# Performance work log

Hardware: AMD Instinct MI355X
Metric: run time of the kernel (lower is better)

The kernel has to match this reference:

```python
import jax, jax.numpy as jnp
import numpy as np

N_NODES = 50000
N_EDGES = 800000
IN_DIM = 128
HID = 64
N_GRAPHS = 256


def setup_inputs() -> dict:
    key = jax.random.key(0)
    ks = jax.random.split(key, 10)
    s = lambda d: 1.0 / np.sqrt(d)
    return {
        'x': jax.random.normal(ks[0], (N_NODES, IN_DIM), jnp.float32),
        'edge_index': jax.random.randint(ks[1], (2, N_EDGES), 0, N_NODES, jnp.int64),
        'batch': jnp.sort(jax.random.randint(ks[2], (N_NODES,), 0, N_GRAPHS, jnp.int64)),
        'Wp': jax.random.normal(ks[3], (IN_DIM, HID), jnp.float32) * s(IN_DIM),
        'bp': jnp.zeros((HID,), jnp.float32),
        'W1_0': jax.random.normal(ks[4], (HID, HID), jnp.float32) * s(HID),
        'b1_0': jnp.zeros((HID,), jnp.float32),
        'W2_0': jax.random.normal(ks[5], (HID, HID), jnp.float32) * s(HID),
        'b2_0': jnp.zeros((HID,), jnp.float32),
        'W1_1': jax.random.normal(ks[6], (HID, HID), jnp.float32) * s(HID),
        'b1_1': jnp.zeros((HID,), jnp.float32),
        'W2_1': jax.random.normal(ks[7], (HID, HID), jnp.float32) * s(HID),
        'b2_1': jnp.zeros((HID,), jnp.float32),
    }


def _gin_layer(h, src, dst, W1, b1, W2, b2):
    # scatter-add aggregation: sum_{j in N(i)} h_j  (messages flow src -> dst)
    agg = jax.ops.segment_sum(h[src], dst, num_segments=N_NODES)
    z = h + agg  # eps = 0 (GINConv default)
    z = jax.nn.relu(z @ W1 + b1)
    z = z @ W2 + b2
    return jax.nn.relu(z)  # outer activation from SharedGINEncoder


def reference(x, edge_index, batch, Wp, bp, W1_0, b1_0, W2_0, b2_0, W1_1, b1_1, W2_1, b2_1):
    src, dst = edge_index[0], edge_index[1]
    h = jax.nn.relu(x @ Wp + bp)  # [N, HID]
    h = _gin_layer(h, src, dst, W1_0, b1_0, W2_0, b2_0)
    h = _gin_layer(h, src, dst, W1_1, b1_1, W2_1, b2_1)
    # global_mean_pool over graph ids
    sums = jax.ops.segment_sum(h, batch, num_segments=N_GRAPHS)  # [G, HID]
    counts = jax.ops.segment_sum(jnp.ones((h.shape[0],), h.dtype), batch, num_segments=N_GRAPHS)
    return sums / jnp.maximum(counts, 1.0)[:, None]
```

## Files before the change

### kernel.cpp

```cpp
#include <hip/hip_runtime.h>

#define N_NODES 50000
#define N_EDGES 800000
#define IN_DIM 128
#define HID 64
#define N_GRAPHS 256

#define E_PER_BLK 4000
#define F_BLOCKS (N_EDGES / E_PER_BLK)
#define NBKT ((N_NODES + 255) / 256)
#define CNT_N (NBKT * F_BLOCKS)
#define SCB ((CNT_N + 255) / 256)
#define NTILES (N_NODES / 4)
#define MTILES (N_NODES / 16)


__device__ __forceinline__ float bf2f(unsigned short v) {
  return __uint_as_float(((unsigned int)v) << 16);
}
__device__ __forceinline__ unsigned short f2bf(float f) {
  unsigned int u = __float_as_uint(f);
  return (unsigned short)((u + 0x7fffu + ((u >> 16) & 1u)) >> 16);
}

typedef __attribute__((ext_vector_type(8))) short bf16x8;
typedef __attribute__((ext_vector_type(4))) float f32x4;

__global__ __launch_bounds__(256) void part_hist_kernel(const int* __restrict__ dst,
                                                        int* __restrict__ cnt) {
  __shared__ int h[NBKT];
  const int t = threadIdx.x;
  for (int k = t; k < NBKT; k += 256) h[k] = 0;
  __syncthreads();
  const int base = blockIdx.x * E_PER_BLK;
  for (int i = t; i < E_PER_BLK; i += 256) atomicAdd(&h[dst[base + i] >> 8], 1);
  __syncthreads();
  for (int k = t; k < NBKT; k += 256) cnt[k * F_BLOCKS + blockIdx.x] = h[k];
}

__global__ __launch_bounds__(256) void scan1g_kernel(const int* __restrict__ in,
                                                     int* __restrict__ ex,
                                                     int* __restrict__ bsum, int n) {
  __shared__ int s[256];
  const int t = threadIdx.x;
  const int i = blockIdx.x * 256 + t;
  int v = (i < n) ? in[i] : 0;
  s[t] = v;
  __syncthreads();
#pragma unroll
  for (int ofs = 1; ofs < 256; ofs <<= 1) {
    int u = (t >= ofs) ? s[t - ofs] : 0;
    __syncthreads();
    s[t] += u;
    __syncthreads();
  }
  if (i < n) ex[i] = s[t] - v;
  if (t == 255) bsum[blockIdx.x] = s[255];
}

__global__ __launch_bounds__(256) void scan2g_kernel(const int* __restrict__ bsum,
                                                     int* __restrict__ bpref, int nb) {
  __shared__ int s[256];
  const int t = threadIdx.x;
  int v = (t < nb) ? bsum[t] : 0;
  s[t] = v;
  __syncthreads();
#pragma unroll
  for (int ofs = 1; ofs < 256; ofs <<= 1) {
    int u = (t >= ofs) ? s[t - ofs] : 0;
    __syncthreads();
    s[t] += u;
    __syncthreads();
  }
  if (t < nb) bpref[t] = s[t] - v;
}

__global__ __launch_bounds__(256) void scan3g_kernel(int* __restrict__ ex,
                                                     const int* __restrict__ bpref, int n) {
  const int i = blockIdx.x * 256 + threadIdx.x;
  if (i < n) ex[i] += bpref[blockIdx.x];
}

__global__ __launch_bounds__(256) void part_scatter_kernel(const int* __restrict__ src,
                                                           const int* __restrict__ dst,
                                                           const int* __restrict__ cex,
                                                           int* __restrict__ psrc,
                                                           int* __restrict__ pdst) {
  __shared__ int cur[NBKT];
  const int t = threadIdx.x;
  for (int k = t; k < NBKT; k += 256) cur[k] = cex[k * F_BLOCKS + blockIdx.x];
  __syncthreads();
  const int base = blockIdx.x * E_PER_BLK;
  for (int i = t; i < E_PER_BLK; i += 256) {
    int d = dst[base + i], s = src[base + i];
    int p = atomicAdd(&cur[d >> 8], 1);
    pdst[p] = d;
    psrc[p] = s;
  }
}

__global__ __launch_bounds__(256) void bucket_sort_kernel(const int* __restrict__ psrc,
                                                          const int* __restrict__ pdst,
                                                          const int* __restrict__ cex,
                                                          int* __restrict__ csr,
                                                          int* __restrict__ off) {
  const int k = blockIdx.x;
  const int t = threadIdx.x;
  const int b0 = cex[k * F_BLOCKS];
  const int b1 = (k == NBKT - 1) ? N_EDGES : cex[(k + 1) * F_BLOCKS];
  __shared__ int cnt[256];
  __shared__ int s[256];
  __shared__ int cur[256];
  cnt[t] = 0;
  __syncthreads();
  for (int i = b0 + t; i < b1; i += 256) atomicAdd(&cnt[pdst[i] & 255], 1);
  __syncthreads();
  int v = cnt[t];
  s[t] = v;
  __syncthreads();
#pragma unroll
  for (int ofs = 1; ofs < 256; ofs <<= 1) {
    int u = (t >= ofs) ? s[t - ofs] : 0;
    __syncthreads();
    s[t] += u;
    __syncthreads();
  }
  const int node = (k << 8) + t;
  const int start = b0 + s[t] - v;
  cur[t] = start;
  if (node < N_NODES) off[node] = start;
  if (k == NBKT - 1 && t == 0) off[N_NODES] = N_EDGES;
  __syncthreads();
  for (int i = b0 + t; i < b1; i += 256) {
    int d = pdst[i];
    int p = atomicAdd(&cur[d & 255], 1);
    csr[p] = psrc[i];
  }
}

__global__ __launch_bounds__(256) void proj_kernel(
    const float* __restrict__ x, const float* __restrict__ Wp,
    const float* __restrict__ bp, unsigned short* __restrict__ h) {
  __shared__ __align__(16) float sX[2][2][4][64];
  __shared__ __align__(16) float sPart[2][2][4][64];
  const int wave = threadIdx.x >> 6, lane = threadIdx.x & 63;
  const int pair = wave >> 1, khalf = wave & 1;
  float w[64];
#pragma unroll
  for (int k = 0; k < 64; ++k) w[k] = Wp[(khalf * 64 + k) * HID + lane];
  const float bias = bp[lane];
  const int pv = blockIdx.x * 2 + pair;
  const int np = gridDim.x * 2;
  const int iters = (NTILES - blockIdx.x * 2 + np - 1) / np;
  for (int it = 0; it < iters; ++it) {
    const int tile = pv + it * np;
    const bool act = (tile < NTILES);
    const int n0 = tile * 4;
    const int buf = it & 1;
    if (act) {
#pragma unroll
      for (int t = 0; t < 4; ++t)
        sX[pair][khalf][t][lane] = x[(n0 + t) * IN_DIM + khalf * 64 + lane];
    }
    float p[4];
#pragma unroll
    for (int t = 0; t < 4; ++t) {
      float a0 = khalf ? 0.f : bias, a1 = 0.f, a2 = 0.f, a3 = 0.f;
#pragma unroll
      for (int k = 0; k < 64; k += 4) {
        float4 v = *(const float4*)&sX[pair][khalf][t][k];
        a0 = fmaf(v.x, w[k + 0], a0);
        a1 = fmaf(v.y, w[k + 1], a1);
        a2 = fmaf(v.z, w[k + 2], a2);
        a3 = fmaf(v.w, w[k + 3], a3);
      }
      p[t] = (a0 + a1) + (a2 + a3);
    }
    if (act && khalf) {
#pragma unroll
      for (int t = 0; t < 4; ++t) sPart[pair][buf][t][lane] = p[t];
    }
    __syncthreads();
    if (act && !khalf) {
#pragma unroll
      for (int t = 0; t < 4; ++t)
        h[(n0 + t) * HID + lane] = f2bf(fmaxf(p[t] + sPart[pair][buf][t][lane], 0.0f));
    }
  }
}

__global__ __launch_bounds__(256) void gather_kernel(
    const unsigned short* __restrict__ h, const int* __restrict__ off,
    const int* __restrict__ csr, unsigned short* __restrict__ agg) {
  const unsigned int* __restrict__ h2 = (const unsigned int*)h;
  unsigned int* __restrict__ agg2 = (unsigned int*)agg;
  const int lane = threadIdx.x & 63;
  const int half = lane >> 5;
  const int c = lane & 31;
  const int wv = (blockIdx.x * 256 + threadIdx.x) >> 6;
  const int nw = (gridDim.x * 256) >> 6;
  for (int n = wv; n < N_NODES; n += nw) {
    const int o0 = off[n], o1 = off[n + 1];
    float ax0 = 0.f, ay0 = 0.f, ax1 = 0.f, ay1 = 0.f;
    float ax2 = 0.f, ay2 = 0.f, ax3 = 0.f, ay3 = 0.f;
    float ax4 = 0.f, ay4 = 0.f, ax5 = 0.f, ay5 = 0.f;
    float ax6 = 0.f, ay6 = 0.f, ax7 = 0.f, ay7 = 0.f;
    if (half == 0) {
      unsigned int u = h2[n * 32 + c];
      ax0 = bf2f((unsigned short)(u & 0xffff));
      ay0 = bf2f((unsigned short)(u >> 16));
    }
    for (int base = o0; base < o1; base += 64) {
      const int cnt = min(64, o1 - base);
      int idxv = (lane < cnt) ? csr[base + lane] : 0;
      int k = 0;
      for (; k + 16 <= cnt; k += 16) {
        int i0 = __shfl(idxv, k + 0 + half);
        int i1 = __shfl(idxv, k + 2 + half);
        int i2 = __shfl(idxv, k + 4 + half);
        int i3 = __shfl(idxv, k + 6 + half);
        int i4 = __shfl(idxv, k + 8 + half);
        int i5 = __shfl(idxv, k + 10 + half);
        int i6 = __shfl(idxv, k + 12 + half);
        int i7 = __shfl(idxv, k + 14 + half);
        unsigned int u0 = h2[i0 * 32 + c];
        unsigned int u1 = h2[i1 * 32 + c];
        unsigned int u2 = h2[i2 * 32 + c];
        unsigned int u3 = h2[i3 * 32 + c];
        unsigned int u4 = h2[i4 * 32 + c];
        unsigned int u5 = h2[i5 * 32 + c];
        unsigned int u6 = h2[i6 * 32 + c];
        unsigned int u7 = h2[i7 * 32 + c];
        ax0 += bf2f((unsigned short)(u0 & 0xffff)); ay0 += bf2f((unsigned short)(u0 >> 16));
        ax1 += bf2f((unsigned short)(u1 & 0xffff)); ay1 += bf2f((unsigned short)(u1 >> 16));
        ax2 += bf2f((unsigned short)(u2 & 0xffff)); ay2 += bf2f((unsigned short)(u2 >> 16));
        ax3 += bf2f((unsigned short)(u3 & 0xffff)); ay3 += bf2f((unsigned short)(u3 >> 16));
        ax4 += bf2f((unsigned short)(u4 & 0xffff)); ay4 += bf2f((unsigned short)(u4 >> 16));
        ax5 += bf2f((unsigned short)(u5 & 0xffff)); ay5 += bf2f((unsigned short)(u5 >> 16));
        ax6 += bf2f((unsigned short)(u6 & 0xffff)); ay6 += bf2f((unsigned short)(u6 >> 16));
        ax7 += bf2f((unsigned short)(u7 & 0xffff)); ay7 += bf2f((unsigned short)(u7 >> 16));
      }
      for (; k < cnt; k += 2) {
        int ke = k + half;
        int ie = __shfl(idxv, (ke < cnt) ? ke : k);
        unsigned int u = h2[ie * 32 + c];
        if (ke < cnt) {
          ax0 += bf2f((unsigned short)(u & 0xffff));
          ay0 += bf2f((unsigned short)(u >> 16));
        }
      }
    }
    float sx = ((ax0 + ax1) + (ax2 + ax3)) + ((ax4 + ax5) + (ax6 + ax7));
    float sy = ((ay0 + ay1) + (ay2 + ay3)) + ((ay4 + ay5) + (ay6 + ay7));
    sx += __shfl_xor(sx, 32);
    sy += __shfl_xor(sy, 32);
    if (half == 0)
      agg2[n * 32 + c] = (unsigned int)f2bf(sx) | ((unsigned int)f2bf(sy) << 16);
  }
}

__global__ __launch_bounds__(256) void mlp_mfma_kernel(
    const unsigned short* __restrict__ agg, const float* __restrict__ W1,
    const float* __restrict__ b1, const float* __restrict__ W2,
    const float* __restrict__ b2, unsigned short* __restrict__ out) {
  __shared__ __align__(16) unsigned short sW1[4096];
  __shared__ __align__(16) unsigned short sW2[4096];
  __shared__ __align__(16) unsigned short sT[4][16][72];
  const int t = threadIdx.x;
  for (int i = t; i < 4096; i += 256) {
    const int k = i >> 6, j = i & 63;
    const int pos = (((j >> 4) * 2 + (k >> 5)) * 64 + ((k >> 3) & 3) * 16 + (j & 15)) * 8 + (k & 7);
    sW1[pos] = f2bf(W1[i]);
    sW2[pos] = f2bf(W2[i]);
  }
  __syncthreads();
  const int wave = t >> 6, lane = t & 63;
  const int row = lane & 15;
  const int kgrp = lane >> 4;
  float bias1[4], bias2[4];
#pragma unroll
  for (int nc = 0; nc < 4; ++nc) {
    bias1[nc] = b1[nc * 16 + row];
    bias2[nc] = b2[nc * 16 + row];
  }
  const int wtile = blockIdx.x * 4 + wave;
  const int ntile = gridDim.x * 4;
  for (int tile = wtile; tile < MTILES; tile += ntile) {
    const int n0 = tile * 16;
    bf16x8 a1[2];
    a1[0] = *(const bf16x8*)&agg[(n0 + row) * HID + kgrp * 8];
    a1[1] = *(const bf16x8*)&agg[(n0 + row) * HID + 32 + kgrp * 8];
    f32x4 acc;
#pragma unroll
    for (int nc = 0; nc < 4; ++nc) {
      acc = (f32x4){bias1[nc], bias1[nc], bias1[nc], bias1[nc]};
#pragma unroll
      for (int ks = 0; ks < 2; ++ks) {
        bf16x8 bf = *(const bf16x8*)&sW1[((nc * 2 + ks) * 64 + lane) * 8];
        acc = __builtin_amdgcn_mfma_f32_16x16x32_bf16(a1[ks], bf, acc, 0, 0, 0);
      }
#pragma unroll
      for (int r = 0; r < 4; ++r)
        sT[wave][kgrp * 4 + r][nc * 16 + row] = f2bf(fmaxf(acc[r], 0.0f));
    }
    bf16x8 a2[2];
    a2[0] = *(const bf16x8*)&sT[wave][row][kgrp * 8];
    a2[1] = *(const bf16x8*)&sT[wave][row][32 + kgrp * 8];
#pragma unroll
    for (int nc = 0; nc < 4; ++nc) {
      acc = (f32x4){bias2[nc], bias2[nc], bias2[nc], bias2[nc]};
#pragma unroll
      for (int ks = 0; ks < 2; ++ks) {
        bf16x8 bf = *(const bf16x8*)&sW2[((nc * 2 + ks) * 64 + lane) * 8];
        acc = __builtin_amdgcn_mfma_f32_16x16x32_bf16(a2[ks], bf, acc, 0, 0, 0);
      }
#pragma unroll
      for (int r = 0; r < 4; ++r)
        sT[wave][kgrp * 4 + r][nc * 16 + row] = f2bf(fmaxf(acc[r], 0.0f));
    }
#pragma unroll
    for (int p = 0; p < 2; ++p) {
      const int idx = p * 64 + lane;
      const int ri = idx >> 3, ch = idx & 7;
      uint4 v = *(const uint4*)&sT[wave][ri][ch * 8];
      *(uint4*)&out[(n0 + ri) * HID + ch * 8] = v;
    }
  }
}

__global__ __launch_bounds__(256) void pool_kernel(const unsigned short* __restrict__ h,
                                                   const int* __restrict__ batch,
                                                   float* __restrict__ out) {
  const int g = blockIdx.x;
  int lo = 0, hi = N_NODES;
  while (lo < hi) {
    int mid = (lo + hi) >> 1;
    if (batch[mid] < g) lo = mid + 1; else hi = mid;
  }
  const int s = lo;
  hi = N_NODES;
  while (lo < hi) {
    int mid = (lo + hi) >> 1;
    if (batch[mid] < g + 1) lo = mid + 1; else hi = mid;
  }
  const int e = lo;
  const int wave = threadIdx.x >> 6, lane = threadIdx.x & 63;
  float a0 = 0.f, a1 = 0.f, a2 = 0.f, a3 = 0.f;
  int n = s + wave;
  for (; n + 12 < e; n += 16) {
    a0 += bf2f(h[n * HID + lane]);
    a1 += bf2f(h[(n + 4) * HID + lane]);
    a2 += bf2f(h[(n + 8) * HID + lane]);
    a3 += bf2f(h[(n + 12) * HID + lane]);
  }
  for (; n < e; n += 4) a0 += bf2f(h[n * HID + lane]);
  __shared__ float red[4][HID];
  red[wave][lane] = ((a0 + a1) + (a2 + a3));
  __syncthreads();
  if (wave == 0) {
    float v = red[0][lane] + red[1][lane] + red[2][lane] + red[3][lane];
    float cnt = (float)(e - s);
    out[g * HID + lane] = v / fmaxf(cnt, 1.0f);
  }
}

extern "C" void kernel_launch(void* const* d_in, const int* in_sizes, int n_in,
                              void* d_out, int out_size, void* d_ws, size_t ws_size,
                              hipStream_t stream) {
  const float* x    = (const float*)d_in[0];
  const int*   edge = (const int*)d_in[1];
  const int*   batch= (const int*)d_in[2];
  const float* Wp   = (const float*)d_in[3];
  const float* bp   = (const float*)d_in[4];
  const float* W1_0 = (const float*)d_in[5];
  const float* b1_0 = (const float*)d_in[6];
  const float* W2_0 = (const float*)d_in[7];
  const float* b2_0 = (const float*)d_in[8];
  const float* W1_1 = (const float*)d_in[9];
  const float* b1_1 = (const float*)d_in[10];
  const float* W2_1 = (const float*)d_in[11];
  const float* b2_1 = (const float*)d_in[12];
  const int* src = edge;
  const int* dst = edge + N_EDGES;
  float* out = (float*)d_out;

  const size_t NB = (size_t)N_NODES * HID;
  unsigned short* hA = (unsigned short*)d_ws;
  unsigned short* hB = hA + NB;
  int* off     = (int*)(hB + NB);
  int* cnt     = off + N_NODES + 1;
  int* cex     = cnt + CNT_N;
  int* sbsum   = cex + CNT_N;
  int* sbpref  = sbsum + SCB;
  int* pdst    = sbpref + SCB;
  int* psrc    = pdst + N_EDGES;
  int* csr     = psrc + N_EDGES;

  dim3 b256(256);

  part_hist_kernel<<<F_BLOCKS, b256, 0, stream>>>(dst, cnt);
  scan1g_kernel<<<SCB, b256, 0, stream>>>(cnt, cex, sbsum, CNT_N);
  scan2g_kernel<<<1, b256, 0, stream>>>(sbsum, sbpref, SCB);
  scan3g_kernel<<<SCB, b256, 0, stream>>>(cex, sbpref, CNT_N);
  part_scatter_kernel<<<F_BLOCKS, b256, 0, stream>>>(src, dst, cex, psrc, pdst);
  bucket_sort_kernel<<<NBKT, b256, 0, stream>>>(psrc, pdst, cex, csr, off);

  proj_kernel<<<2048, b256, 0, stream>>>(x, Wp, bp, hA);

  gather_kernel<<<12500, b256, 0, stream>>>(hA, off, csr, hB);
  mlp_mfma_kernel<<<256, b256, 0, stream>>>(hB, W1_0, b1_0, W2_0, b2_0, hB);

  gather_kernel<<<12500, b256, 0, stream>>>(hB, off, csr, hA);
  mlp_mfma_kernel<<<256, b256, 0, stream>>>(hA, W1_1, b1_1, W2_1, b2_1, hA);

  pool_kernel<<<N_GRAPHS, b256, 0, stream>>>(hA, batch, out);
}
```

Baseline: 140.8 us.

## Fuse neighbor gather into MFMA MLP kernel and fold scan fixup into consumers

```diff
diff --git a/kernel.cpp b/kernel.cpp
--- a/kernel.cpp
+++ b/kernel.cpp
@@ -75,20 +75,18 @@
   if (t < nb) bpref[t] = s[t] - v;
 }
 
-__global__ __launch_bounds__(256) void scan3g_kernel(int* __restrict__ ex,
-                                                     const int* __restrict__ bpref, int n) {
-  const int i = blockIdx.x * 256 + threadIdx.x;
-  if (i < n) ex[i] += bpref[blockIdx.x];
-}
-
 __global__ __launch_bounds__(256) void part_scatter_kernel(const int* __restrict__ src,
                                                            const int* __restrict__ dst,
                                                            const int* __restrict__ cex,
+                                                           const int* __restrict__ bpref,
                                                            int* __restrict__ psrc,
                                                            int* __restrict__ pdst) {
   __shared__ int cur[NBKT];
   const int t = threadIdx.x;
-  for (int k = t; k < NBKT; k += 256) cur[k] = cex[k * F_BLOCKS + blockIdx.x];
+  for (int k = t; k < NBKT; k += 256) {
+    const int i = k * F_BLOCKS + blockIdx.x;
+    cur[k] = cex[i] + bpref[i >> 8];
+  }
   __syncthreads();
   const int base = blockIdx.x * E_PER_BLK;
   for (int i = t; i < E_PER_BLK; i += 256) {
@@ -102,12 +100,18 @@
 __global__ __launch_bounds__(256) void bucket_sort_kernel(const int* __restrict__ psrc,
                                                           const int* __restrict__ pdst,
                                                           const int* __restrict__ cex,
+                                                          const int* __restrict__ bpref,
                                                           int* __restrict__ csr,
                                                           int* __restrict__ off) {
   const int k = blockIdx.x;
   const int t = threadIdx.x;
-  const int b0 = cex[k * F_BLOCKS];
-  const int b1 = (k == NBKT - 1) ? N_EDGES : cex[(k + 1) * F_BLOCKS];
+  const int i0 = k * F_BLOCKS;
+  const int b0 = cex[i0] + bpref[i0 >> 8];
+  int b1 = N_EDGES;
+  if (k != NBKT - 1) {
+    const int i1 = (k + 1) * F_BLOCKS;
+    b1 = cex[i1] + bpref[i1 >> 8];
+  }
   __shared__ int cnt[256];
   __shared__ int s[256];
   __shared__ int cur[256];
@@ -189,80 +193,11 @@
   }
 }
 
-__global__ __launch_bounds__(256) void gather_kernel(
-    const unsigned short* __restrict__ h, const int* __restrict__ off,
-    const int* __restrict__ csr, unsigned short* __restrict__ agg) {
-  const unsigned int* __restrict__ h2 = (const unsigned int*)h;
-  unsigned int* __restrict__ agg2 = (unsigned int*)agg;
-  const int lane = threadIdx.x & 63;
-  const int half = lane >> 5;
-  const int c = lane & 31;
-  const int wv = (blockIdx.x * 256 + threadIdx.x) >> 6;
-  const int nw = (gridDim.x * 256) >> 6;
-  for (int n = wv; n < N_NODES; n += nw) {
-    const int o0 = off[n], o1 = off[n + 1];
-    float ax0 = 0.f, ay0 = 0.f, ax1 = 0.f, ay1 = 0.f;
-    float ax2 = 0.f, ay2 = 0.f, ax3 = 0.f, ay3 = 0.f;
-    float ax4 = 0.f, ay4 = 0.f, ax5 = 0.f, ay5 = 0.f;
-    float ax6 = 0.f, ay6 = 0.f, ax7 = 0.f, ay7 = 0.f;
-    if (half == 0) {
-      unsigned int u = h2[n * 32 + c];
-      ax0 = bf2f((unsigned short)(u & 0xffff));
-      ay0 = bf2f((unsigned short)(u >> 16));
-    }
-    for (int base = o0; base < o1; base += 64) {
-      const int cnt = min(64, o1 - base);
-      int idxv = (lane < cnt) ? csr[base + lane] : 0;
-      int k = 0;
-      for (; k + 16 <= cnt; k += 16) {
-        int i0 = __shfl(idxv, k + 0 + half);
-        int i1 = __shfl(idxv, k + 2 + half);
-        int i2 = __shfl(idxv, k + 4 + half);
-        int i3 = __shfl(idxv, k + 6 + half);
-        int i4 = __shfl(idxv, k + 8 + half);
-        int i5 = __shfl(idxv, k + 10 + half);
-        int i6 = __shfl(idxv, k + 12 + half);
-        int i7 = __shfl(idxv, k + 14 + half);
-        unsigned int u0 = h2[i0 * 32 + c];
-        unsigned int u1 = h2[i1 * 32 + c];
-        unsigned int u2 = h2[i2 * 32 + c];
-        unsigned int u3 = h2[i3 * 32 + c];
-        unsigned int u4 = h2[i4 * 32 + c];
-        unsigned int u5 = h2[i5 * 32 + c];
-        unsigned int u6 = h2[i6 * 32 + c];
-        unsigned int u7 = h2[i7 * 32 + c];
-        ax0 += bf2f((unsigned short)(u0 & 0xffff)); ay0 += bf2f((unsigned short)(u0 >> 16));
-        ax1 += bf2f((unsigned short)(u1 & 0xffff)); ay1 += bf2f((unsigned short)(u1 >> 16));
-        ax2 += bf2f((unsigned short)(u2 & 0xffff)); ay2 += bf2f((unsigned short)(u2 >> 16));
-        ax3 += bf2f((unsigned short)(u3 & 0xffff)); ay3 += bf2f((unsigned short)(u3 >> 16));
-        ax4 += bf2f((unsigned short)(u4 & 0xffff)); ay4 += bf2f((unsigned short)(u4 >> 16));
-        ax5 += bf2f((unsigned short)(u5 & 0xffff)); ay5 += bf2f((unsigned short)(u5 >> 16));
-        ax6 += bf2f((unsigned short)(u6 & 0xffff)); ay6 += bf2f((unsigned short)(u6 >> 16));
-        ax7 += bf2f((unsigned short)(u7 & 0xffff)); ay7 += bf2f((unsigned short)(u7 >> 16));
-      }
-      for (; k < cnt; k += 2) {
-        int ke = k + half;
-        int ie = __shfl(idxv, (ke < cnt) ? ke : k);
-        unsigned int u = h2[ie * 32 + c];
-        if (ke < cnt) {
-          ax0 += bf2f((unsigned short)(u & 0xffff));
-          ay0 += bf2f((unsigned short)(u >> 16));
-        }
-      }
-    }
-    float sx = ((ax0 + ax1) + (ax2 + ax3)) + ((ax4 + ax5) + (ax6 + ax7));
-    float sy = ((ay0 + ay1) + (ay2 + ay3)) + ((ay4 + ay5) + (ay6 + ay7));
-    sx += __shfl_xor(sx, 32);
-    sy += __shfl_xor(sy, 32);
-    if (half == 0)
-      agg2[n * 32 + c] = (unsigned int)f2bf(sx) | ((unsigned int)f2bf(sy) << 16);
-  }
-}
-
-__global__ __launch_bounds__(256) void mlp_mfma_kernel(
-    const unsigned short* __restrict__ agg, const float* __restrict__ W1,
+__global__ __launch_bounds__(256) void gin_fused_mfma_kernel(
+    const unsigned short* __restrict__ h_in, const int* __restrict__ off,
+    const int* __restrict__ csr, const float* __restrict__ W1,
     const float* __restrict__ b1, const float* __restrict__ W2,
-    const float* __restrict__ b2, unsigned short* __restrict__ out) {
+    const float* __restrict__ b2, unsigned short* __restrict__ h_out) {
   __shared__ __align__(16) unsigned short sW1[4096];
   __shared__ __align__(16) unsigned short sW2[4096];
   __shared__ __align__(16) unsigned short sT[4][16][72];
@@ -283,13 +218,59 @@
     bias1[nc] = b1[nc * 16 + row];
     bias2[nc] = b2[nc * 16 + row];
   }
-  const int wtile = blockIdx.x * 4 + wave;
-  const int ntile = gridDim.x * 4;
-  for (int tile = wtile; tile < MTILES; tile += ntile) {
+  const uint4* __restrict__ hv = (const uint4*)h_in;
+  const int tile = blockIdx.x * 4 + wave;
+  if (tile < MTILES) {
     const int n0 = tile * 16;
+    const int n = n0 + row;
+    const int o0 = off[n];
+    const int deg = off[n + 1] - o0;
+    int dm = deg;
+#pragma unroll
+    for (int m = 1; m <= 8; m <<= 1) {
+      int o = __shfl_xor(dm, m);
+      dm = (o > dm) ? o : dm;
+    }
+    float ac0[8], ac1[8];
+    {
+      uint4 ua = hv[n * 8 + kgrp];
+      uint4 ub = hv[n * 8 + 4 + kgrp];
+      const unsigned int* pa = (const unsigned int*)&ua;
+      const unsigned int* pb = (const unsigned int*)&ub;
+#pragma unroll
+      for (int e = 0; e < 4; ++e) {
+        ac0[2 * e] = bf2f((unsigned short)(pa[e] & 0xffff));
+        ac0[2 * e + 1] = bf2f((unsigned short)(pa[e] >> 16));
+        ac1[2 * e] = bf2f((unsigned short)(pb[e] & 0xffff));
+        ac1[2 * e + 1] = bf2f((unsigned short)(pb[e] >> 16));
+      }
+    }
+    for (int j = 0; j < dm; j += 4) {
+#pragma unroll
+      for (int u = 0; u < 4; ++u) {
+        const int jj = j + u;
+        const int pos = o0 + ((jj < deg) ? jj : 0);
+        const int idx = csr[(pos < N_EDGES) ? pos : (N_EDGES - 1)];
+        const float m = (jj < deg) ? 1.0f : 0.0f;
+        uint4 ua = hv[idx * 8 + kgrp];
+        uint4 ub = hv[idx * 8 + 4 + kgrp];
+        const unsigned int* pa = (const unsigned int*)&ua;
+        const unsigned int* pb = (const unsigned int*)&ub;
+#pragma unroll
+        for (int e = 0; e < 4; ++e) {
+          ac0[2 * e] = fmaf(m, bf2f((unsigned short)(pa[e] & 0xffff)), ac0[2 * e]);
+          ac0[2 * e + 1] = fmaf(m, bf2f((unsigned short)(pa[e] >> 16)), ac0[2 * e + 1]);
+          ac1[2 * e] = fmaf(m, bf2f((unsigned short)(pb[e] & 0xffff)), ac1[2 * e]);
+          ac1[2 * e + 1] = fmaf(m, bf2f((unsigned short)(pb[e] >> 16)), ac1[2 * e + 1]);
+        }
+      }
+    }
     bf16x8 a1[2];
-    a1[0] = *(const bf16x8*)&agg[(n0 + row) * HID + kgrp * 8];
-    a1[1] = *(const bf16x8*)&agg[(n0 + row) * HID + 32 + kgrp * 8];
+#pragma unroll
+    for (int e = 0; e < 8; ++e) {
+      a1[0][e] = (short)f2bf(ac0[e]);
+      a1[1][e] = (short)f2bf(ac1[e]);
+    }
     f32x4 acc;
 #pragma unroll
     for (int nc = 0; nc < 4; ++nc) {
@@ -320,10 +301,10 @@
     }
 #pragma unroll
     for (int p = 0; p < 2; ++p) {
-      const int idx = p * 64 + lane;
-      const int ri = idx >> 3, ch = idx & 7;
+      const int idx2 = p * 64 + lane;
+      const int ri = idx2 >> 3, ch = idx2 & 7;
       uint4 v = *(const uint4*)&sT[wave][ri][ch * 8];
-      *(uint4*)&out[(n0 + ri) * HID + ch * 8] = v;
+      *(uint4*)&h_out[(n0 + ri) * HID + ch * 8] = v;
     }
   }
 }
@@ -401,17 +382,13 @@
   part_hist_kernel<<<F_BLOCKS, b256, 0, stream>>>(dst, cnt);
   scan1g_kernel<<<SCB, b256, 0, stream>>>(cnt, cex, sbsum, CNT_N);
   scan2g_kernel<<<1, b256, 0, stream>>>(sbsum, sbpref, SCB);
-  scan3g_kernel<<<SCB, b256, 0, stream>>>(cex, sbpref, CNT_N);
-  part_scatter_kernel<<<F_BLOCKS, b256, 0, stream>>>(src, dst, cex, psrc, pdst);
-  bucket_sort_kernel<<<NBKT, b256, 0, stream>>>(psrc, pdst, cex, csr, off);
+  part_scatter_kernel<<<F_BLOCKS, b256, 0, stream>>>(src, dst, cex, sbpref, psrc, pdst);
+  bucket_sort_kernel<<<NBKT, b256, 0, stream>>>(psrc, pdst, cex, sbpref, csr, off);
 
   proj_kernel<<<2048, b256, 0, stream>>>(x, Wp, bp, hA);
 
-  gather_kernel<<<12500, b256, 0, stream>>>(hA, off, csr, hB);
-  mlp_mfma_kernel<<<256, b256, 0, stream>>>(hB, W1_0, b1_0, W2_0, b2_0, hB);
-
-  gather_kernel<<<12500, b256, 0, stream>>>(hB, off, csr, hA);
-  mlp_mfma_kernel<<<256, b256, 0, stream>>>(hA, W1_1, b1_1, W2_1, b2_1, hA);
+  gin_fused_mfma_kernel<<<782, b256, 0, stream>>>(hA, off, csr, W1_0, b1_0, W2_0, b2_0, hB);
+  gin_fused_mfma_kernel<<<782, b256, 0, stream>>>(hB, off, csr, W1_1, b1_1, W2_1, b2_1, hA);
 
   pool_kernel<<<N_GRAPHS, b256, 0, stream>>>(hA, batch, out);
 }
```

Result: no change. 140.8 us (+0.0%).
